# Kernel tuning notes

Hardware: AMD Instinct MI355X
Metric: run time of the kernel (lower is better)

## Reference

```python
import jax, jax.numpy as jnp
import numpy as np

B, S, D, H = 2, 2048, 1024, 16
DK = D // H


def setup_inputs() -> dict:
    key = jax.random.key(0)
    ks = jax.random.split(key, 12)
    scale = 1.0 / np.sqrt(D)
    inp = {
        "q": jax.random.normal(ks[0], (B, S, D), dtype=jnp.float32),
        "k": jax.random.normal(ks[1], (B, S, D), dtype=jnp.float32),
        "v": jax.random.normal(ks[2], (B, S, D), dtype=jnp.float32),
        "mask": jax.random.randint(ks[3], (B, 1, 1, S), 0, 2, dtype=jnp.int32),
        "Wq": jax.random.normal(ks[4], (D, D), dtype=jnp.float32) * scale,
        "bq": jnp.zeros((D,), dtype=jnp.float32),
        "Wk": jax.random.normal(ks[5], (D, D), dtype=jnp.float32) * scale,
        "bk": jnp.zeros((D,), dtype=jnp.float32),
        "Wv": jax.random.normal(ks[6], (D, D), dtype=jnp.float32) * scale,
        "bv": jnp.zeros((D,), dtype=jnp.float32),
        "Wo": jax.random.normal(ks[7], (D, D), dtype=jnp.float32) * scale,
        "bo": jnp.zeros((D,), dtype=jnp.float32),
    }
    return inp


def reference(q, k, v, mask, Wq, bq, Wk, bk, Wv, bv, Wo, bo):
    # Linear projections (torch nn.Linear: x @ W.T + b)
    query = q @ Wq.T + bq                      # [B,S,D]
    key = k @ Wk.T + bk
    value = v @ Wv.T + bv
    # split heads -> [B,H,S,DK]
    def split(x):
        return x.reshape(B, S, H, DK).transpose(0, 2, 1, 3)
    qh, kh, vh = split(query), split(key), split(value)
    # scaled dot-product attention with additive mask
    scores = jnp.einsum("bhqd,bhkd->bhqk", qh, kh) / jnp.sqrt(jnp.float32(DK))
    scores = jnp.where(mask == 0, jnp.float32(-1e9), scores)
    attn = jax.nn.softmax(scores, axis=-1)     # [B,H,S,S]
    out = jnp.einsum("bhqk,bhkd->bhqd", attn, vh)
    out = out.transpose(0, 2, 1, 3).reshape(B, S, D)
    return out @ Wo.T + bo
```

## Files before the change

kernel.cpp:

```cpp
#include <hip/hip_runtime.h>


constexpr int BB = 2;
constexpr int SS = 2048;
constexpr int DD = 1024;
constexpr int HH = 16;
constexpr int DKK = 64;

typedef float f32x4 __attribute__((ext_vector_type(4)));
typedef __bf16 bf16x8 __attribute__((ext_vector_type(8)));
typedef short s16x8 __attribute__((ext_vector_type(8)));
typedef short s16x4 __attribute__((ext_vector_type(4)));
typedef unsigned u32x2 __attribute__((ext_vector_type(2)));
typedef unsigned u32x4 __attribute__((ext_vector_type(4)));

#define DEV static __device__ __forceinline__

DEV f32x4 mfma16(s16x8 a, s16x8 b, f32x4 c) {
  return __builtin_amdgcn_mfma_f32_16x16x32_bf16(
      __builtin_bit_cast(bf16x8, a), __builtin_bit_cast(bf16x8, b), c, 0, 0, 0);
}

#if __has_builtin(__builtin_amdgcn_mfma_f32_16x16x16bf16_1k)
DEV f32x4 mfma16k(s16x4 a, s16x4 b, f32x4 c) {
  return __builtin_amdgcn_mfma_f32_16x16x16bf16_1k(a, b, c, 0, 0, 0);
}
#else
DEV f32x4 mfma16k(s16x4 a, s16x4 b, f32x4 c) {
  asm volatile(
      "s_nop 1\n\t"
      "v_mfma_f32_16x16x16_bf16 %0, %1, %2, %0\n\t"
      "s_nop 7\n\t"
      "s_nop 7"
      : "+v"(c)
      : "v"(a), "v"(b));
  return c;
}
#endif

DEV void split1(float x, short& h, short& l) {
  unsigned u = __float_as_uint(x);
  h = (short)(u >> 16);
  float hf = __uint_as_float(u & 0xffff0000u);
  l = (short)(__float_as_uint(x - hf) >> 16);
}
DEV short f2bf_rne(float x) {
  unsigned u = __float_as_uint(x);
  return (short)((u + 0x7fffu + ((u >> 16) & 1u)) >> 16);
}
DEV unsigned cvtpk(float lo, float hi) {
  unsigned r;
  asm("v_cvt_pk_bf16_f32 %0, %1, %2" : "=v"(r) : "v"(lo), "v"(hi));
  return r;
}
DEV s16x8 load8s(const short* p) { return *(const s16x8*)p; }

DEV void gld_lds16(const short* g, short* l) {
  __builtin_amdgcn_global_load_lds(
      (const __attribute__((address_space(1))) void*)g,
      (__attribute__((address_space(3))) void*)l, 16, 0, 0);
}

DEV int vperm(int s_t, int d) {
  const int sub = (s_t >> 4) & 3, qd = (s_t >> 2) & 3, j = s_t & 3;
  const int slot = (((qd << 1) | (sub >> 1)) ^ (d & 7));
  return (slot << 3) | ((sub & 1) << 2) | j;
}

DEV void split4(const float* __restrict__ X, short* __restrict__ H,
                short* __restrict__ L, int i) {
  float4 x = *(const float4*)(X + i);
  float xs[4] = {x.x, x.y, x.z, x.w};
  s16x4 h4, l4;
#pragma unroll
  for (int e = 0; e < 4; ++e) {
    short h, l;
    split1(xs[e], h, l);
    h4[e] = h;
    l4[e] = l;
  }
  *(s16x4*)(H + i) = h4;
  *(s16x4*)(L + i) = l4;
}

DEV void cast4(const float* __restrict__ X, short* __restrict__ Y, int i) {
  float4 x = *(const float4*)(X + i);
  float xs[4] = {x.x, x.y, x.z, x.w};
  s16x4 y4;
#pragma unroll
  for (int e = 0; e < 4; ++e) y4[e] = f2bf_rne(xs[e]);
  *(s16x4*)(Y + i) = y4;
}

__global__ __launch_bounds__(256) void prep(
    const float* __restrict__ Wq, short* __restrict__ Wqh, short* __restrict__ Wql,
    const float* __restrict__ Wk, short* __restrict__ Wkh, short* __restrict__ Wkl,
    const float* __restrict__ Wo, short* __restrict__ Woh, short* __restrict__ Wol,
    const float* __restrict__ Wv, short* __restrict__ Wvh,
    const float* __restrict__ q, short* __restrict__ qH, short* __restrict__ qL,
    const float* __restrict__ k, short* __restrict__ kH, short* __restrict__ kL) {
  const int bid = blockIdx.x;
  const int t = threadIdx.x;
  if (bid < 4096) {
    const int w = bid >> 10;
    const int i = ((bid & 1023) * 256 + t) * 4;
    if (w == 0) split4(Wq, Wqh, Wql, i);
    else if (w == 1) split4(Wk, Wkh, Wkl, i);
    else if (w == 2) split4(Wo, Woh, Wol, i);
    else cast4(Wv, Wvh, i);
  } else {
    const int a = (bid - 4096) >> 12;
    const int i = (((bid - 4096) & 4095) * 256 + t) * 4;
    if (a == 0) split4(q, qH, qL, i);
    else split4(k, kH, kL, i);
  }
}

__global__ __launch_bounds__(256) void cast_rne(const float* __restrict__ X,
                                                short* __restrict__ Y) {
  int i = (blockIdx.x * 256 + threadIdx.x) * 4;
  cast4(X, Y, i);
}

__global__ __launch_bounds__(256) void gemm_qk(
    const short* __restrict__ qAh, const short* __restrict__ qAl,
    const short* __restrict__ Wqh, const short* __restrict__ Wql,
    const float* __restrict__ bq, short* __restrict__ Qo,
    const short* __restrict__ kAh, const short* __restrict__ kAl,
    const short* __restrict__ Wkh, const short* __restrict__ Wkl,
    const float* __restrict__ bk, short* __restrict__ Kho,
    short* __restrict__ Klo) {
  __shared__ short lds[2][12288];

  const int tid = threadIdx.x;
  const int lane = tid & 63, wv = tid >> 6;
  const int lo16 = lane & 15, quad = lane >> 4;
  const int sel = blockIdx.x >> 9;
  const int bid = blockIdx.x & 511;
  const int m0 = (bid & 31) * 128;
  const int n0 = (bid >> 5) * 64;

  const short* Agh = sel ? kAh : qAh;
  const short* Agl = sel ? kAl : qAl;
  const short* Wgh = sel ? Wkh : Wqh;
  const short* Wgl = sel ? Wkl : Wql;
  const float* bias = sel ? bk : bq;

  f32x4 acc[2][4];
#pragma unroll
  for (int mt = 0; mt < 2; ++mt)
#pragma unroll
    for (int nt = 0; nt < 4; ++nt) acc[mt][nt] = f32x4{0.f, 0.f, 0.f, 0.f};

  const int rw = tid >> 2, qw = tid & 3;
  const int ra0 = tid >> 2, ra1 = (tid + 256) >> 2;

  auto stage = [&](int k0, int buf) {
    short* sAh = lds[buf];
    short* sAl = lds[buf] + 4096;
    short* sWh = lds[buf] + 8192;
    short* sWl = lds[buf] + 10240;
    gld_lds16(Wgh + (size_t)(n0 + rw) * DD + k0 + qw * 8, sWh + tid * 8);
    gld_lds16(Wgl + (size_t)(n0 + rw) * DD + k0 + qw * 8, sWl + tid * 8);
    gld_lds16(Agh + (size_t)(m0 + ra0) * DD + k0 + qw * 8, sAh + tid * 8);
    gld_lds16(Agh + (size_t)(m0 + ra1) * DD + k0 + qw * 8, sAh + (tid + 256) * 8);
    if (sel) {
      gld_lds16(Agl + (size_t)(m0 + ra0) * DD + k0 + qw * 8, sAl + tid * 8);
      gld_lds16(Agl + (size_t)(m0 + ra1) * DD + k0 + qw * 8, sAl + (tid + 256) * 8);
    }
  };

  stage(0, 0);

  for (int kk = 0; kk < DD / 32; ++kk) {
    __syncthreads();
    if (kk + 1 < DD / 32) stage((kk + 1) * 32, (kk + 1) & 1);

    const short* sAh = lds[kk & 1];
    const short* sAl = lds[kk & 1] + 4096;
    const short* sWh = lds[kk & 1] + 8192;
    const short* sWl = lds[kk & 1] + 10240;

    s16x8 ah[2], al[2], wh[4], wl[4];
#pragma unroll
    for (int mt = 0; mt < 2; ++mt) {
      const int r = wv * 32 + mt * 16 + lo16;
      ah[mt] = *(const s16x8*)&sAh[r * 32 + quad * 8];
      if (sel) al[mt] = *(const s16x8*)&sAl[r * 32 + quad * 8];
    }
#pragma unroll
    for (int nt = 0; nt < 4; ++nt) {
      const int r = nt * 16 + lo16;
      wh[nt] = *(const s16x8*)&sWh[r * 32 + quad * 8];
      wl[nt] = *(const s16x8*)&sWl[r * 32 + quad * 8];
    }
#pragma unroll
    for (int mt = 0; mt < 2; ++mt)
#pragma unroll
      for (int nt = 0; nt < 4; ++nt) {
        acc[mt][nt] = mfma16(ah[mt], wh[nt], acc[mt][nt]);
        acc[mt][nt] = mfma16(ah[mt], wl[nt], acc[mt][nt]);
        if (sel) acc[mt][nt] = mfma16(al[mt], wh[nt], acc[mt][nt]);
      }
  }

#pragma unroll
  for (int mt = 0; mt < 2; ++mt)
#pragma unroll
    for (int nt = 0; nt < 4; ++nt) {
      const int n = n0 + nt * 16 + lo16;
      const float bv = bias[n];
#pragma unroll
      for (int r = 0; r < 4; ++r) {
        const int m = m0 + wv * 32 + mt * 16 + quad * 4 + r;
        const float val = acc[mt][nt][r] + bv;
        const int b = m >> 11, s = m & 2047;
        const int h = n >> 6, dk = n & 63;
        if (sel == 0) {
          size_t idx = ((size_t)(b * HH + h) * SS + s) * DKK + dk;
          Qo[idx] = f2bf_rne(val);
        } else {
          const int dk_sw = dk ^ ((s & 7) << 3);
          size_t idx = ((size_t)(b * HH + h) * SS + s) * DKK + dk_sw;
          short hh, ll;
          split1(val, hh, ll);
          Kho[idx] = hh;
          Klo[idx] = ll;
        }
      }
    }
}

template <int SPLIT, int EPI>
__global__ __launch_bounds__(256) void gemm_tile(
    const short* __restrict__ Agh,
    const short* __restrict__ Wgh, const short* __restrict__ Wgl,
    const float* __restrict__ bias, void* __restrict__ O1) {
  __shared__ short lds[2][12288];

  const int tid = threadIdx.x;
  const int lane = tid & 63, wv = tid >> 6;
  const int lo16 = lane & 15, quad = lane >> 4;
  const int m0 = (blockIdx.x & 31) * 128;
  const int n0 = (blockIdx.x >> 5) * 64;

  f32x4 acc[2][4];
#pragma unroll
  for (int mt = 0; mt < 2; ++mt)
#pragma unroll
    for (int nt = 0; nt < 4; ++nt) acc[mt][nt] = f32x4{0.f, 0.f, 0.f, 0.f};

  const int rw = tid >> 2, qw = tid & 3;
  const int ra0 = tid >> 2, ra1 = (tid + 256) >> 2;

  auto stage = [&](int k0, int buf) {
    short* sAh = lds[buf];
    short* sWh = lds[buf] + 8192;
    short* sWl = lds[buf] + 10240;
    gld_lds16(Wgh + (size_t)(n0 + rw) * DD + k0 + qw * 8, sWh + tid * 8);
    if constexpr (SPLIT == 2)
      gld_lds16(Wgl + (size_t)(n0 + rw) * DD + k0 + qw * 8, sWl + tid * 8);
    gld_lds16(Agh + (size_t)(m0 + ra0) * DD + k0 + qw * 8, sAh + tid * 8);
    gld_lds16(Agh + (size_t)(m0 + ra1) * DD + k0 + qw * 8, sAh + (tid + 256) * 8);
  };

  stage(0, 0);

  for (int kk = 0; kk < DD / 32; ++kk) {
    __syncthreads();
    if (kk + 1 < DD / 32) stage((kk + 1) * 32, (kk + 1) & 1);

    const short* sAh = lds[kk & 1];
    const short* sWh = lds[kk & 1] + 8192;
    const short* sWl = lds[kk & 1] + 10240;

    s16x8 ah[2], wh[4], wl[4];
#pragma unroll
    for (int mt = 0; mt < 2; ++mt) {
      const int r = wv * 32 + mt * 16 + lo16;
      ah[mt] = *(const s16x8*)&sAh[r * 32 + quad * 8];
    }
#pragma unroll
    for (int nt = 0; nt < 4; ++nt) {
      const int r = nt * 16 + lo16;
      wh[nt] = *(const s16x8*)&sWh[r * 32 + quad * 8];
      if constexpr (SPLIT == 2) wl[nt] = *(const s16x8*)&sWl[r * 32 + quad * 8];
    }
#pragma unroll
    for (int mt = 0; mt < 2; ++mt)
#pragma unroll
      for (int nt = 0; nt < 4; ++nt) {
        acc[mt][nt] = mfma16(ah[mt], wh[nt], acc[mt][nt]);
        if constexpr (SPLIT == 2)
          acc[mt][nt] = mfma16(ah[mt], wl[nt], acc[mt][nt]);
      }
  }

#pragma unroll
  for (int mt = 0; mt < 2; ++mt)
#pragma unroll
    for (int nt = 0; nt < 4; ++nt) {
      const int n = n0 + nt * 16 + lo16;
      const float bv = bias[n];
#pragma unroll
      for (int r = 0; r < 4; ++r) {
        const int m = m0 + wv * 32 + mt * 16 + quad * 4 + r;
        const float val = acc[mt][nt][r] + bv;
        const int b = m >> 11, s = m & 2047;
        const int h = n >> 6, dk = n & 63;
        if constexpr (EPI == 1) {
          const int col = (s & ~63) | vperm(s & 63, dk);
          size_t idx = ((size_t)(b * HH + h) * DKK + dk) * SS + col;
          ((short*)O1)[idx] = f2bf_rne(val);
        } else {
          ((float*)O1)[(size_t)m * DD + n] = val;
        }
      }
    }
}

constexpr int NKB = SS / 64;
constexpr float EXPSC = 0.125f * 1.4426950408889634f;

__global__ __launch_bounds__(256, 2) void mha_attn(
    const short* __restrict__ Qh, const short* __restrict__ Kh,
    const short* __restrict__ Kl, const short* __restrict__ Vt,
    const int* __restrict__ mask, short* __restrict__ Ao) {
  __shared__ __align__(16) short sKV[2][12288];

  const int tid = threadIdx.x;
  const int lane = tid & 63, wv = tid >> 6;
  const int lo16 = lane & 15, quad = lane >> 4;
  const int bid = blockIdx.x;
  const int head = (bid & 7) * 4 + ((bid >> 3) & 3);
  const int qblk = bid >> 5;
  const int q0 = qblk * 128 + wv * 32;
  const int b = head >> 4;

  const size_t hbase = (size_t)head * SS;
  const size_t vbase = (size_t)head * DKK;

  constexpr short ONE_BF = (short)0x3F80;
  const s16x4 ones4 = {ONE_BF, ONE_BF, ONE_BF, ONE_BF};

  s16x8 qh[2][2];
#pragma unroll
  for (int rt = 0; rt < 2; ++rt) {
    size_t qb = (hbase + q0 + rt * 16 + lo16) * DKK + quad * 8;
#pragma unroll
    for (int c = 0; c < 2; ++c) qh[rt][c] = load8s(Qh + qb + c * 32);
  }

  f32x4 Oacc[2][4];
#pragma unroll
  for (int rt = 0; rt < 2; ++rt)
#pragma unroll
    for (int t = 0; t < 4; ++t) Oacc[rt][t] = f32x4{0.f, 0.f, 0.f, 0.f};
  f32x4 sacc[2];
  sacc[0] = f32x4{0.f, 0.f, 0.f, 0.f};
  sacc[1] = f32x4{0.f, 0.f, 0.f, 0.f};

  auto STAGE = [&](int k0, int buf) {
    short* base = &sKV[buf][0];
#pragma unroll
    for (int i = 0; i < 2; ++i) {
      const int ch = tid + 256 * i;
      const int row = ch >> 3;
      const int inner = (ch & 7) * 8;
      gld_lds16(Kh + (hbase + k0 + row) * DKK + inner, base + ch * 8);
      gld_lds16(Kl + (hbase + k0 + row) * DKK + inner, base + 4096 + ch * 8);
      gld_lds16(Vt + (vbase + row) * SS + k0 + inner, base + 8192 + ch * 8);
    }
  };

  STAGE(0, 0);

  for (int kb = 0; kb < NKB; ++kb) {
    const int k0g = kb * 64;
    const int cur = kb & 1;
    __syncthreads();

    if (kb + 1 < NKB) STAGE(k0g + 64, cur ^ 1);

    const short* sKh = &sKV[cur][0];
    const short* sKl = &sKV[cur][4096];
    const short* sV = &sKV[cur][8192];

    float addf[4][4];
#pragma unroll
    for (int sub = 0; sub < 4; ++sub) {
      const int4 mq = *(const int4*)(mask + b * SS + k0g + sub * 16 + quad * 4);
      addf[sub][0] = mq.x ? 0.f : -32768.f;
      addf[sub][1] = mq.y ? 0.f : -32768.f;
      addf[sub][2] = mq.z ? 0.f : -32768.f;
      addf[sub][3] = mq.w ? 0.f : -32768.f;
    }

    f32x4 sc4[2][4];
    __builtin_amdgcn_s_setprio(1);
#pragma unroll
    for (int sub = 0; sub < 4; ++sub) {
      sc4[0][sub] = f32x4{0.f, 0.f, 0.f, 0.f};
      sc4[1][sub] = f32x4{0.f, 0.f, 0.f, 0.f};
      const int krow = sub * 16 + lo16;
      const int ksw = (krow & 7) << 3;
#pragma unroll
      for (int c = 0; c < 2; ++c) {
        const int koff = krow * 64 + ((c * 32 + quad * 8) ^ ksw);
        s16x8 kh = *(const s16x8*)&sKh[koff];
        s16x8 kl = *(const s16x8*)&sKl[koff];
#pragma unroll
        for (int rt = 0; rt < 2; ++rt) {
          sc4[rt][sub] = mfma16(kh, qh[rt][c], sc4[rt][sub]);
          sc4[rt][sub] = mfma16(kl, qh[rt][c], sc4[rt][sub]);
        }
      }
    }
    __builtin_amdgcn_s_setprio(0);

    s16x4 pb[2][4];
#pragma unroll
    for (int rt = 0; rt < 2; ++rt)
#pragma unroll
      for (int sub = 0; sub < 4; ++sub) {
        const float p0 = exp2f(fmaf(sc4[rt][sub][0], EXPSC, addf[sub][0]));
        const float p1 = exp2f(fmaf(sc4[rt][sub][1], EXPSC, addf[sub][1]));
        const float p2 = exp2f(fmaf(sc4[rt][sub][2], EXPSC, addf[sub][2]));
        const float p3 = exp2f(fmaf(sc4[rt][sub][3], EXPSC, addf[sub][3]));
        u32x2 w;
        w[0] = cvtpk(p0, p1);
        w[1] = cvtpk(p2, p3);
        pb[rt][sub] = __builtin_bit_cast(s16x4, w);
      }

    __builtin_amdgcn_s_setprio(1);
#pragma unroll
    for (int rt = 0; rt < 2; ++rt)
#pragma unroll
      for (int sub = 0; sub < 4; ++sub)
        sacc[rt] = mfma16k(ones4, pb[rt][sub], sacc[rt]);
#pragma unroll
    for (int t = 0; t < 4; ++t) {
      const int vrow = t * 16 + lo16;
#pragma unroll
      for (int h2 = 0; h2 < 2; ++h2) {
        const int slot = (((quad << 1) | h2) ^ (vrow & 7));
        s16x8 va8 = *(const s16x8*)&sV[vrow * 64 + slot * 8];
        s16x4 va0 = {va8[0], va8[1], va8[2], va8[3]};
        s16x4 va1 = {va8[4], va8[5], va8[6], va8[7]};
#pragma unroll
        for (int rt = 0; rt < 2; ++rt) {
          Oacc[rt][t] = mfma16k(va0, pb[rt][2 * h2], Oacc[rt][t]);
          Oacc[rt][t] = mfma16k(va1, pb[rt][2 * h2 + 1], Oacc[rt][t]);
        }
      }
    }
    __builtin_amdgcn_s_setprio(0);
  }

  __syncthreads();
  float* sT = (float*)&sKV[0][0] + wv * (16 * 68);
  const int h = head & 15;
#pragma unroll
  for (int rt = 0; rt < 2; ++rt) {
    const float rinv = 1.0f / sacc[rt][0];
#pragma unroll
    for (int t = 0; t < 4; ++t) {
      f32x4 vv;
#pragma unroll
      for (int r = 0; r < 4; ++r) vv[r] = Oacc[rt][t][r] * rinv;
      *(f32x4*)&sT[lo16 * 68 + t * 16 + quad * 4] = vv;
    }
#pragma unroll
    for (int i = 0; i < 4; ++i) {
      const int qrow = quad + 4 * i;
      f32x4 vv = *(const f32x4*)&sT[qrow * 68 + lo16 * 4];
      const int row = q0 + rt * 16 + qrow;
      const size_t idx = ((size_t)b * SS + row) * DD + h * DKK + lo16 * 4;
      u32x2 w;
      w[0] = cvtpk(vv[0], vv[1]);
      w[1] = cvtpk(vv[2], vv[3]);
      *(s16x4*)&Ao[idx] = __builtin_bit_cast(s16x4, w);
    }
  }
}

extern "C" void kernel_launch(void* const* d_in, const int* in_sizes, int n_in,
                              void* d_out, int out_size, void* d_ws, size_t ws_size,
                              hipStream_t stream) {
  const float* q = (const float*)d_in[0];
  const float* k = (const float*)d_in[1];
  const float* v = (const float*)d_in[2];
  const int* mask = (const int*)d_in[3];
  const float* Wq = (const float*)d_in[4];
  const float* bq = (const float*)d_in[5];
  const float* Wk = (const float*)d_in[6];
  const float* bk = (const float*)d_in[7];
  const float* Wv = (const float*)d_in[8];
  const float* bv = (const float*)d_in[9];
  const float* Wo = (const float*)d_in[10];
  const float* bo = (const float*)d_in[11];

  char* ws = (char*)d_ws;
  size_t off = 0;
  auto take = [&](size_t bytes) {
    char* p = ws + off;
    off += (bytes + 255) & ~(size_t)255;
    return p;
  };
  const size_t WE = (size_t)DD * DD;
  const size_t TE = (size_t)BB * SS * DD;

  short* Wqh = (short*)take(WE * 2);
  short* Wql = (short*)take(WE * 2);
  short* Wkh = (short*)take(WE * 2);
  short* Wkl = (short*)take(WE * 2);
  short* Wvh = (short*)take(WE * 2);
  short* Woh = (short*)take(WE * 2);
  short* Wol = (short*)take(WE * 2);
  short* qH = (short*)take(TE * 2);
  short* qL = (short*)take(TE * 2);
  short* kH = (short*)take(TE * 2);
  short* kL = (short*)take(TE * 2);
  short* Qh = (short*)take(TE * 2);
  short* Kh = (short*)take(TE * 2);
  short* Kl = (short*)take(TE * 2);
  (void)ws_size;
  short* vH = qH;
  short* Vt = qL;
  short* Ao = kH;

  prep<<<12288, 256, 0, stream>>>(Wq, Wqh, Wql, Wk, Wkh, Wkl, Wo, Woh, Wol,
                                  Wv, Wvh, q, qH, qL, k, kH, kL);

  gemm_qk<<<1024, 256, 0, stream>>>(qH, qL, Wqh, Wql, bq, Qh,
                                    kH, kL, Wkh, Wkl, bk, Kh, Kl);

  cast_rne<<<4096, 256, 0, stream>>>(v, vH);
  gemm_tile<0, 1><<<512, 256, 0, stream>>>(vH, Wvh, nullptr, bv, Vt);

  mha_attn<<<512, 256, 0, stream>>>(Qh, Kh, Kl, Vt, mask, Ao);

  gemm_tile<2, 2><<<512, 256, 0, stream>>>(Ao, Woh, Wol, bo, d_out);
}
```

Baseline: 287.1 us.

## Fuse V cast into prep, drop unused q low split, widen QK GEMM N-tile

The prep kernel now also casts v to bf16, removing the separate cast_rne launch. q is only rounded to bf16 because its low half was never used in the MFMA sum, which saves writing one split buffer. The Q/K projection GEMM tile goes from 128x64 to 128x128 with half as many blocks, so each A-tile load is reused across twice as many N columns. The cost is doubled accumulator registers and larger LDS, which may lower occupancy, and only 512 blocks are launched.

```diff
diff --git a/kernel.cpp b/kernel.cpp
--- a/kernel.cpp
+++ b/kernel.cpp
@@ -12,7 +12,6 @@
 typedef short s16x8 __attribute__((ext_vector_type(8)));
 typedef short s16x4 __attribute__((ext_vector_type(4)));
 typedef unsigned u32x2 __attribute__((ext_vector_type(2)));
-typedef unsigned u32x4 __attribute__((ext_vector_type(4)));
 
 #define DEV static __device__ __forceinline__
 
@@ -97,8 +96,9 @@
     const float* __restrict__ Wk, short* __restrict__ Wkh, short* __restrict__ Wkl,
     const float* __restrict__ Wo, short* __restrict__ Woh, short* __restrict__ Wol,
     const float* __restrict__ Wv, short* __restrict__ Wvh,
-    const float* __restrict__ q, short* __restrict__ qH, short* __restrict__ qL,
-    const float* __restrict__ k, short* __restrict__ kH, short* __restrict__ kL) {
+    const float* __restrict__ q, short* __restrict__ qH,
+    const float* __restrict__ k, short* __restrict__ kH, short* __restrict__ kL,
+    const float* __restrict__ v, short* __restrict__ vH) {
   const int bid = blockIdx.x;
   const int t = threadIdx.x;
   if (bid < 4096) {
@@ -108,65 +108,63 @@
     else if (w == 1) split4(Wk, Wkh, Wkl, i);
     else if (w == 2) split4(Wo, Woh, Wol, i);
     else cast4(Wv, Wvh, i);
+  } else if (bid < 8192) {
+    const int i = ((bid - 4096) * 256 + t) * 4;
+    cast4(q, qH, i);
+  } else if (bid < 12288) {
+    const int i = ((bid - 8192) * 256 + t) * 4;
+    split4(k, kH, kL, i);
   } else {
-    const int a = (bid - 4096) >> 12;
-    const int i = (((bid - 4096) & 4095) * 256 + t) * 4;
-    if (a == 0) split4(q, qH, qL, i);
-    else split4(k, kH, kL, i);
-  }
-}
-
-__global__ __launch_bounds__(256) void cast_rne(const float* __restrict__ X,
-                                                short* __restrict__ Y) {
-  int i = (blockIdx.x * 256 + threadIdx.x) * 4;
-  cast4(X, Y, i);
+    const int i = ((bid - 12288) * 256 + t) * 4;
+    cast4(v, vH, i);
+  }
 }
 
 __global__ __launch_bounds__(256) void gemm_qk(
-    const short* __restrict__ qAh, const short* __restrict__ qAl,
+    const short* __restrict__ qAh,
     const short* __restrict__ Wqh, const short* __restrict__ Wql,
     const float* __restrict__ bq, short* __restrict__ Qo,
     const short* __restrict__ kAh, const short* __restrict__ kAl,
     const short* __restrict__ Wkh, const short* __restrict__ Wkl,
     const float* __restrict__ bk, short* __restrict__ Kho,
     short* __restrict__ Klo) {
-  __shared__ short lds[2][12288];
+  __shared__ short lds[2][16384];
 
   const int tid = threadIdx.x;
   const int lane = tid & 63, wv = tid >> 6;
   const int lo16 = lane & 15, quad = lane >> 4;
-  const int sel = blockIdx.x >> 9;
-  const int bid = blockIdx.x & 511;
+  const int sel = blockIdx.x >> 8;
+  const int bid = blockIdx.x & 255;
   const int m0 = (bid & 31) * 128;
-  const int n0 = (bid >> 5) * 64;
+  const int n0 = (bid >> 5) * 128;
 
   const short* Agh = sel ? kAh : qAh;
-  const short* Agl = sel ? kAl : qAl;
   const short* Wgh = sel ? Wkh : Wqh;
   const short* Wgl = sel ? Wkl : Wql;
   const float* bias = sel ? bk : bq;
 
-  f32x4 acc[2][4];
+  f32x4 acc[2][8];
 #pragma unroll
   for (int mt = 0; mt < 2; ++mt)
 #pragma unroll
-    for (int nt = 0; nt < 4; ++nt) acc[mt][nt] = f32x4{0.f, 0.f, 0.f, 0.f};
-
-  const int rw = tid >> 2, qw = tid & 3;
-  const int ra0 = tid >> 2, ra1 = (tid + 256) >> 2;
+    for (int nt = 0; nt < 8; ++nt) acc[mt][nt] = f32x4{0.f, 0.f, 0.f, 0.f};
+
+  const int ra0 = tid >> 2, ra1 = (tid >> 2) + 64, qw = tid & 3;
 
   auto stage = [&](int k0, int buf) {
     short* sAh = lds[buf];
     short* sAl = lds[buf] + 4096;
     short* sWh = lds[buf] + 8192;
-    short* sWl = lds[buf] + 10240;
-    gld_lds16(Wgh + (size_t)(n0 + rw) * DD + k0 + qw * 8, sWh + tid * 8);
-    gld_lds16(Wgl + (size_t)(n0 + rw) * DD + k0 + qw * 8, sWl + tid * 8);
+    short* sWl = lds[buf] + 12288;
+    gld_lds16(Wgh + (size_t)(n0 + ra0) * DD + k0 + qw * 8, sWh + tid * 8);
+    gld_lds16(Wgh + (size_t)(n0 + ra1) * DD + k0 + qw * 8, sWh + (tid + 256) * 8);
+    gld_lds16(Wgl + (size_t)(n0 + ra0) * DD + k0 + qw * 8, sWl + tid * 8);
+    gld_lds16(Wgl + (size_t)(n0 + ra1) * DD + k0 + qw * 8, sWl + (tid + 256) * 8);
     gld_lds16(Agh + (size_t)(m0 + ra0) * DD + k0 + qw * 8, sAh + tid * 8);
     gld_lds16(Agh + (size_t)(m0 + ra1) * DD + k0 + qw * 8, sAh + (tid + 256) * 8);
     if (sel) {
-      gld_lds16(Agl + (size_t)(m0 + ra0) * DD + k0 + qw * 8, sAl + tid * 8);
-      gld_lds16(Agl + (size_t)(m0 + ra1) * DD + k0 + qw * 8, sAl + (tid + 256) * 8);
+      gld_lds16(kAl + (size_t)(m0 + ra0) * DD + k0 + qw * 8, sAl + tid * 8);
+      gld_lds16(kAl + (size_t)(m0 + ra1) * DD + k0 + qw * 8, sAl + (tid + 256) * 8);
     }
   };
 
@@ -179,9 +177,9 @@
     const short* sAh = lds[kk & 1];
     const short* sAl = lds[kk & 1] + 4096;
     const short* sWh = lds[kk & 1] + 8192;
-    const short* sWl = lds[kk & 1] + 10240;
-
-    s16x8 ah[2], al[2], wh[4], wl[4];
+    const short* sWl = lds[kk & 1] + 12288;
+
+    s16x8 ah[2], al[2];
 #pragma unroll
     for (int mt = 0; mt < 2; ++mt) {
       const int r = wv * 32 + mt * 16 + lo16;
@@ -189,25 +187,23 @@
       if (sel) al[mt] = *(const s16x8*)&sAl[r * 32 + quad * 8];
     }
 #pragma unroll
-    for (int nt = 0; nt < 4; ++nt) {
+    for (int nt = 0; nt < 8; ++nt) {
       const int r = nt * 16 + lo16;
-      wh[nt] = *(const s16x8*)&sWh[r * 32 + quad * 8];
-      wl[nt] = *(const s16x8*)&sWl[r * 32 + quad * 8];
-    }
-#pragma unroll
-    for (int mt = 0; mt < 2; ++mt)
-#pragma unroll
-      for (int nt = 0; nt < 4; ++nt) {
-        acc[mt][nt] = mfma16(ah[mt], wh[nt], acc[mt][nt]);
-        acc[mt][nt] = mfma16(ah[mt], wl[nt], acc[mt][nt]);
-        if (sel) acc[mt][nt] = mfma16(al[mt], wh[nt], acc[mt][nt]);
-      }
+      s16x8 wh = *(const s16x8*)&sWh[r * 32 + quad * 8];
+      s16x8 wl = *(const s16x8*)&sWl[r * 32 + quad * 8];
+#pragma unroll
+      for (int mt = 0; mt < 2; ++mt) {
+        acc[mt][nt] = mfma16(ah[mt], wh, acc[mt][nt]);
+        acc[mt][nt] = mfma16(ah[mt], wl, acc[mt][nt]);
+        if (sel) acc[mt][nt] = mfma16(al[mt], wh, acc[mt][nt]);
+      }
+    }
   }
 
 #pragma unroll
   for (int mt = 0; mt < 2; ++mt)
 #pragma unroll
-    for (int nt = 0; nt < 4; ++nt) {
+    for (int nt = 0; nt < 8; ++nt) {
       const int n = n0 + nt * 16 + lo16;
       const float bv = bias[n];
 #pragma unroll
@@ -519,24 +515,22 @@
   short* Woh = (short*)take(WE * 2);
   short* Wol = (short*)take(WE * 2);
   short* qH = (short*)take(TE * 2);
-  short* qL = (short*)take(TE * 2);
+  short* vH = (short*)take(TE * 2);
   short* kH = (short*)take(TE * 2);
   short* kL = (short*)take(TE * 2);
   short* Qh = (short*)take(TE * 2);
   short* Kh = (short*)take(TE * 2);
   short* Kl = (short*)take(TE * 2);
   (void)ws_size;
-  short* vH = qH;
-  short* Vt = qL;
+  short* Vt = qH;
   short* Ao = kH;
 
-  prep<<<12288, 256, 0, stream>>>(Wq, Wqh, Wql, Wk, Wkh, Wkl, Wo, Woh, Wol,
-                                  Wv, Wvh, q, qH, qL, k, kH, kL);
-
-  gemm_qk<<<1024, 256, 0, stream>>>(qH, qL, Wqh, Wql, bq, Qh,
-                                    kH, kL, Wkh, Wkl, bk, Kh, Kl);
-
-  cast_rne<<<4096, 256, 0, stream>>>(v, vH);
+  prep<<<16384, 256, 0, stream>>>(Wq, Wqh, Wql, Wk, Wkh, Wkl, Wo, Woh, Wol,
+                                  Wv, Wvh, q, qH, k, kH, kL, v, vH);
+
+  gemm_qk<<<512, 256, 0, stream>>>(qH, Wqh, Wql, bq, Qh,
+                                   kH, kL, Wkh, Wkl, bk, Kh, Kl);
+
   gemm_tile<0, 1><<<512, 256, 0, stream>>>(vH, Wvh, nullptr, bv, Vt);
 
   mha_attn<<<512, 256, 0, stream>>>(Qh, Kh, Kl, Vt, mask, Ao);
```

After: 280.4 us. 2.3% less time.
